# Kernel tuning notes

Hardware: AMD Instinct MI355X
Metric: run time of the kernel (lower is better)

## Reference

```python
import jax, jax.numpy as jnp
import numpy as np

NPOINT, NSAMPLE, RADIUS = 2048, 32, 0.2
EPS = 1e-5


def setup_inputs() -> dict:
    key = jax.random.key(0)
    ks = jax.random.split(key, 12)
    B, N, C = 8, 8192, 64
    mlp = [64, 64, 128]
    inp = {
        "xyz": jax.random.normal(ks[0], (B, 3, N), dtype=jnp.float32),
        "points": jax.random.normal(ks[1], (B, C, N), dtype=jnp.float32),
    }
    last = C + 3  # use_xyz concatenates 3 relative coords
    for i, out in enumerate(mlp, 1):
        inp[f"W{i}"] = jax.random.normal(ks[2 * i], (out, last), dtype=jnp.float32) / np.sqrt(last).astype(np.float32)
        inp[f"b{i}"] = jnp.zeros((out,), jnp.float32)
        inp[f"g{i}"] = jnp.ones((out,), jnp.float32)
        inp[f"be{i}"] = jnp.zeros((out,), jnp.float32)
        last = out
    return inp


def fps(xyz_t, npoint):
    """Farthest point sampling. xyz_t: (B,N,3) -> (B,npoint) int32 indices."""
    xyz_t = jax.lax.stop_gradient(xyz_t)  # indices are non-differentiable
    B, N, _ = xyz_t.shape

    def step(carry, _):
        dists, far = carry  # (B,N), (B,)
        cent = jnp.take_along_axis(xyz_t, far[:, None, None], axis=1)  # (B,1,3)
        d = jnp.sum((xyz_t - cent) ** 2, axis=-1)
        dists = jnp.minimum(dists, d)
        nf = jnp.argmax(dists, axis=-1).astype(jnp.int32)
        return (dists, nf), far

    init = (jnp.full((B, N), 1e10, xyz_t.dtype), jnp.zeros((B,), jnp.int32))
    _, idxs = jax.lax.scan(step, init, None, length=npoint)
    return jnp.transpose(idxs)  # (B, npoint)


def ball_query(xyz_t, new_xyz_t, radius, nsample):
    """First-nsample-in-radius neighbor indices, padded with first hit.
    xyz_t (B,N,3), new_xyz_t (B,M,3) -> (B,M,nsample) int32."""
    B, N, _ = xyz_t.shape
    # squared distances via gemm to avoid (B,M,N,3) intermediate
    sq = (jnp.sum(new_xyz_t ** 2, -1)[:, :, None]
          + jnp.sum(xyz_t ** 2, -1)[:, None, :]
          - 2.0 * jnp.einsum('bmd,bnd->bmn', new_xyz_t, xyz_t))  # (B,M,N)
    cand = jnp.where(sq < radius * radius, jnp.arange(N, dtype=jnp.int32), N)
    idx = jnp.sort(cand, axis=-1)[:, :, :nsample]  # first k in-radius by index order
    first = idx[:, :, :1]
    first = jnp.where(first == N, 0, first)  # guard empty groups
    idx = jnp.where(idx == N, first, idx)
    return idx


def group(feat, idx):
    """feat (B,C,N), idx (B,M,k) -> (B,C,M,k) gathered neighbor features."""
    return jnp.take_along_axis(feat[:, :, None, :], idx[:, None, :, :], axis=3)


def conv_bn_relu(x, W, b, g, be):
    """Shared 1x1 Conv2d + BatchNorm2d (batch stats, training mode) + ReLU.
    x: (B,C,M,K) -> (B,O,M,K)."""
    y = jnp.einsum('oc,bcmk->bomk', W, x) + b[None, :, None, None]
    mu = jnp.mean(y, axis=(0, 2, 3), keepdims=True)
    var = jnp.var(y, axis=(0, 2, 3), keepdims=True)
    y = (y - mu) * jax.lax.rsqrt(var + EPS)
    y = y * g[None, :, None, None] + be[None, :, None, None]
    return jax.nn.relu(y)


def reference(xyz, points, W1, b1, g1, be1, W2, b2, g2, be2, W3, b3, g3, be3):
    xyz_t = jnp.transpose(xyz, (0, 2, 1))  # (B,N,3)
    fidx = fps(xyz_t, NPOINT)  # (B,M)
    new_xyz = jnp.take_along_axis(xyz, fidx[:, None, :], axis=2)  # (B,3,M)
    idx = ball_query(xyz_t, jnp.transpose(new_xyz, (0, 2, 1)), RADIUS, NSAMPLE)  # (B,M,K)
    grouped_xyz = group(xyz, idx) - new_xyz[:, :, :, None]  # (B,3,M,K) centered
    grouped_pts = group(points, idx)  # (B,f,M,K)
    x = jnp.concatenate([grouped_xyz, grouped_pts], axis=1)  # (B,f+3,M,K)
    x = conv_bn_relu(x, W1, b1, g1, be1)
    x = conv_bn_relu(x, W2, b2, g2, be2)
    x = conv_bn_relu(x, W3, b3, g3, be3)
    new_points = jnp.max(x, axis=3)  # (B,mlp[-1],M)
    return (new_xyz, new_points)
```

## Files before the change

### kernel.cpp

```cpp
#include <hip/hip_runtime.h>

#define BB 8
#define NN 8192
#define MM 2048
#define KK 32
#define NTOT (BB*MM*KK)

#define WS_PTS_T  0
#define WS_XYZN   4194304
#define WS_IDX    5242880
#define WS_GPART  5767168
#define WS_PARAMS 6291456
#define WS_ZMAX   6292480
#define WS_ZMIN   8389632
#define WS_TOTAL  10486784

typedef float v2f __attribute__((ext_vector_type(2)));

__global__ __launch_bounds__(256) void k_transpose(const float* __restrict__ pts,
                                                   float* __restrict__ pts_t){
  __shared__ float tile[64][65];
  int bid = blockIdx.x;
  int b = bid >> 7;
  int n0 = (bid & 127) << 6;
  int tx = threadIdx.x & 63, ty = threadIdx.x >> 6;
  const float* src = pts + (size_t)b*64*NN;
  #pragma unroll
  for (int c = ty; c < 64; c += 4)
    tile[c][tx] = src[(size_t)c*NN + n0 + tx];
  __syncthreads();
  float* dst = pts_t + ((size_t)b*NN + n0)*64;
  #pragma unroll
  for (int r = ty; r < 64; r += 4)
    dst[(size_t)r*64 + tx] = tile[tx][r];
}

__global__ __launch_bounds__(256) void k_xyzn(const float* __restrict__ xyz,
                                              float4* __restrict__ xyzn){
  #pragma clang fp contract(off)
  int i = blockIdx.x*256 + threadIdx.x;
  int b = i >> 13, n = i & 8191;
  const float* p = xyz + (size_t)b*3*NN;
  float x = p[n], y = p[NN+n], z = p[2*NN+n];
  float nrm = (x*x + y*y) + z*z;
  xyzn[i] = make_float4(x, y, z, nrm);
}

#define DPPMAXF(ctrl, rmask)                                                 \
  {                                                                          \
    float s_ = __int_as_float(__builtin_amdgcn_update_dpp(                   \
        __float_as_int(m), __float_as_int(m), (ctrl), (rmask), 0xf, false)); \
    m = fmaxf(m, s_);                                                        \
  }

__global__ __launch_bounds__(256,1) void k_fps(const float* __restrict__ xyz,
                                               float* __restrict__ out_newxyz){
  #pragma clang fp contract(off)
  __shared__ float4 sp4[NN];
  __shared__ unsigned long long swk[2][4];
  int b = blockIdx.x, tid = threadIdx.x;
  const float* xb = xyz + (size_t)b*3*NN;
  int n0 = tid << 5;
  v2f px[16], py[16], pz[16], dd[16];
  const float4* xb4 = (const float4*)xb;
  #pragma unroll
  for (int q = 0; q < 8; ++q){
    float4 X = xb4[(n0>>2) + q];
    float4 Y = xb4[(NN>>2) + (n0>>2) + q];
    float4 Z = xb4[((2*NN)>>2) + (n0>>2) + q];
    px[2*q]   = (v2f){X.x, X.y}; px[2*q+1] = (v2f){X.z, X.w};
    py[2*q]   = (v2f){Y.x, Y.y}; py[2*q+1] = (v2f){Y.z, Y.w};
    pz[2*q]   = (v2f){Z.x, Z.y}; pz[2*q+1] = (v2f){Z.z, Z.w};
    dd[2*q]   = (v2f){1e10f,1e10f}; dd[2*q+1] = (v2f){1e10f,1e10f};
    sp4[n0+4*q+0] = make_float4(X.x, Y.x, Z.x, 0.f);
    sp4[n0+4*q+1] = make_float4(X.y, Y.y, Z.y, 0.f);
    sp4[n0+4*q+2] = make_float4(X.z, Y.z, Z.z, 0.f);
    sp4[n0+4*q+3] = make_float4(X.w, Y.w, Z.w, 0.f);
  }
  __syncthreads();
  float4 c0 = sp4[0];
  float cx = c0.x, cy = c0.y, cz = c0.z;
  float* ob = out_newxyz + (size_t)b*3*MM;
  int lane = tid & 63, wid = tid >> 6;
  const int JINF = 0x7fffffff;
  for (int s = 0; s < 8; ++s){
    float ox = 0.f, oy = 0.f, oz = 0.f;
    #pragma unroll 1
    for (int ti = 0; ti < 256; ++ti){
      if (tid == ti){ ox = cx; oy = cy; oz = cz; }
      v2f cvx = (v2f){cx,cx}, cvy = (v2f){cy,cy}, cvz = (v2f){cz,cz};
      #pragma unroll
      for (int g = 0; g < 16; ++g){
        v2f dx = px[g]-cvx, dy = py[g]-cvy, dz = pz[g]-cvz;
        v2f xx = dx*dx, yy = dy*dy, zz = dz*dz;
        v2f sm = xx + yy;
        v2f d  = sm + zz;
        dd[g] = __builtin_elementwise_min(dd[g], d);
      }
      v2f t8[8], t4[4], t2[2], t1;
      #pragma unroll
      for (int g = 0; g < 8; ++g) t8[g] = __builtin_elementwise_max(dd[2*g], dd[2*g+1]);
      #pragma unroll
      for (int g = 0; g < 4; ++g) t4[g] = __builtin_elementwise_max(t8[2*g], t8[2*g+1]);
      t2[0] = __builtin_elementwise_max(t4[0], t4[1]);
      t2[1] = __builtin_elementwise_max(t4[2], t4[3]);
      t1 = __builtin_elementwise_max(t2[0], t2[1]);
      float bv = fmaxf(t1.x, t1.y);
      float m = bv;
      DPPMAXF(0x111, 0xf)
      DPPMAXF(0x112, 0xf)
      DPPMAXF(0x114, 0xf)
      DPPMAXF(0x118, 0xf)
      DPPMAXF(0x142, 0xa)
      DPPMAXF(0x143, 0xc)
      float wm = __int_as_float(__builtin_amdgcn_readlane(__float_as_int(m), 63));
      unsigned long long msk = __ballot(bv == wm);
      int wl = (int)__builtin_ctzll(msk);
      int s16[16], s8[8], s4[4], s2[2];
      #pragma unroll
      for (int g = 0; g < 16; ++g){
        int j0 = (dd[g].x == bv) ? (2*g)   : JINF;
        int j1 = (dd[g].y == bv) ? (2*g+1) : JINF;
        s16[g] = min(j0, j1);
      }
      #pragma unroll
      for (int g = 0; g < 8; ++g) s8[g] = min(s16[2*g], s16[2*g+1]);
      #pragma unroll
      for (int g = 0; g < 4; ++g) s4[g] = min(s8[2*g], s8[2*g+1]);
      s2[0] = min(s4[0], s4[1]); s2[1] = min(s4[2], s4[3]);
      int bj = min(s2[0], s2[1]);
      int nwin = __builtin_amdgcn_readlane(n0 + bj, wl);
      int buf = ti & 1;
      if (lane == 0){
        unsigned long long key =
            ((unsigned long long)__float_as_uint(wm) << 32) |
            (unsigned int)(~(unsigned int)nwin);
        swk[buf][wid] = key;
      }
      __syncthreads();
      const unsigned long long* kk = swk[buf];
      unsigned long long k0=kk[0], k1=kk[1], k2=kk[2], k3=kk[3];
      unsigned long long a = (k0>k1)?k0:k1, c2 = (k2>k3)?k2:k3;
      unsigned long long kmax = (a>c2)?a:c2;
      int far = (int)(~(unsigned int)kmax) & (NN-1);
      float4 c4 = sp4[far];
      cx = c4.x; cy = c4.y; cz = c4.z;
    }
    ob[(s<<8)+tid] = ox; ob[MM+(s<<8)+tid] = oy; ob[2*MM+(s<<8)+tid] = oz;
  }
}

__global__ __launch_bounds__(256) void k_ballq(const float4* __restrict__ xyzn,
                                               const float* __restrict__ newxyz,
                                               int* __restrict__ idx){
  #pragma clang fp contract(off)
  __shared__ unsigned long long s_mask[32][129];
  __shared__ float4 s_c4[32];
  const float R2 = (float)(0.2*0.2);
  int b = blockIdx.x >> 6;
  int m0 = (blockIdx.x & 63) << 5;
  int tid = threadIdx.x, lane = tid & 63, wv = tid >> 6;
  const float* nb = newxyz + (size_t)b*3*MM;
  if (tid < 32){
    int m = m0 + tid;
    float cx = nb[m], cy = nb[MM+m], cz = nb[2*MM+m];
    float cn = (cx*cx + cy*cy) + cz*cz;
    s_c4[tid] = make_float4(cx, cy, cz, cn);
  }
  __syncthreads();
  const float4* src = xyzn + (size_t)b*NN;
  for (int ci = 0; ci < 32; ++ci){
    int ch = ci*4 + wv;
    float4 p = src[ch*64 + lane];
    #pragma unroll 8
    for (int mi = 0; mi < 32; ++mi){
      float4 c = s_c4[mi];
      float dot = (c.x*p.x + c.y*p.y) + c.z*p.z;
      float sq = (c.w + p.w) - 2.0f*dot;
      unsigned long long mk = __ballot(sq < R2);
      if (lane == 0) s_mask[mi][ch] = mk;
    }
  }
  __syncthreads();
  if (tid < 32){
    int m = m0 + tid;
    int* om = idx + ((size_t)(b*MM + m))*KK;
    int filled = 0, first = -1;
    for (int ch = 0; ch < 128 && filled < KK; ++ch){
      unsigned long long mk = s_mask[tid][ch];
      while (mk){
        int bp = __builtin_ctzll(mk);
        mk &= mk - 1;
        int j = ch*64 + bp;
        if (first < 0) first = j;
        om[filled++] = j;
        if (filled == KK) break;
      }
    }
    int pad = (first < 0) ? 0 : first;
    for (int s = filled; s < KK; ++s) om[s] = pad;
  }
}

#define XST 260
#define PST 66

__device__ __forceinline__ void gemm_step(v2f (&acc)[8][4], const float* sw,
                                          const float* sx, int c, int ob8, int pb){
  float4 X0 = *(const float4*)&sx[c*XST + pb];
  float4 X1 = *(const float4*)&sx[c*XST + pb + 4];
  v2f xv[4] = { (v2f){X0.x,X0.y}, (v2f){X0.z,X0.w},
                (v2f){X1.x,X1.y}, (v2f){X1.z,X1.w} };
  float4 W0 = *(const float4*)&sw[c*64 + ob8];
  float4 W1 = *(const float4*)&sw[c*64 + ob8 + 4];
  float ws[8] = {W0.x,W0.y,W0.z,W0.w,W1.x,W1.y,W1.z,W1.w};
  #pragma unroll
  for (int oi = 0; oi < 8; ++oi){
    v2f wv = (v2f){ws[oi], ws[oi]};
    #pragma unroll
    for (int p = 0; p < 4; ++p)
      acc[oi][p] = __builtin_elementwise_fma(wv, xv[p], acc[oi][p]);
  }
}

__device__ __forceinline__ void zero_acc(v2f (&acc)[8][4]){
  #pragma unroll
  for (int oi = 0; oi < 8; ++oi)
    #pragma unroll
    for (int p = 0; p < 4; ++p) acc[oi][p] = (v2f){0.f, 0.f};
}

__device__ __forceinline__ void gather_col(float* sx, const float* pts_t,
    const float4* xyzn, const float* nb, const int* idx, int b, int bid, int tid){
  int m0 = (bid & 255) << 3;
  int m = m0 + (tid >> 5), k = tid & 31;
  int j = idx[((size_t)(b*MM + m))*KK + k];
  float4 P = xyzn[(size_t)b*NN + j];
  sx[0*XST + tid] = P.x - nb[m];
  sx[1*XST + tid] = P.y - nb[MM+m];
  sx[2*XST + tid] = P.z - nb[2*MM+m];
  const float4* pf = (const float4*)(pts_t + ((size_t)b*NN + j)*64);
  #pragma unroll
  for (int c4 = 0; c4 < 16; ++c4){
    float4 v = pf[c4];
    sx[(3+4*c4+0)*XST + tid] = v.x;
    sx[(3+4*c4+1)*XST + tid] = v.y;
    sx[(3+4*c4+2)*XST + tid] = v.z;
    sx[(3+4*c4+3)*XST + tid] = v.w;
  }
}

__device__ __forceinline__ void bnrelu_tile(v2f (&acc)[8][4], const float* sA,
                                            const float* sC, int ob8){
  v2f Z = (v2f){0.f, 0.f};
  #pragma unroll
  for (int oi = 0; oi < 8; ++oi){
    v2f Av = (v2f){sA[ob8+oi], sA[ob8+oi]};
    v2f Cv = (v2f){sC[ob8+oi], sC[ob8+oi]};
    #pragma unroll
    for (int p = 0; p < 4; ++p)
      acc[oi][p] = __builtin_elementwise_max(
          __builtin_elementwise_fma(Av, acc[oi][p], Cv), Z);
  }
}

__device__ __forceinline__ void stash_tile(const v2f (&acc)[8][4], float* sx,
                                           int ob8, int pb){
  #pragma unroll
  for (int oi = 0; oi < 8; ++oi){
    *(float4*)&sx[(ob8+oi)*XST + pb] =
        make_float4(acc[oi][0].x, acc[oi][0].y, acc[oi][1].x, acc[oi][1].y);
    *(float4*)&sx[(ob8+oi)*XST + pb + 4] =
        make_float4(acc[oi][2].x, acc[oi][2].y, acc[oi][3].x, acc[oi][3].y);
  }
}

__device__ __forceinline__ void tile_stats(const v2f (&acc)[8][4], float* s_pp,
    float* gpart, int ob8, int pg, int tid, int bid, int nch_base){
  #pragma unroll
  for (int oi = 0; oi < 8; ++oi){
    float a0x=acc[oi][0].x, a0y=acc[oi][0].y, a0z=acc[oi][1].x, a0w=acc[oi][1].y;
    float a1x=acc[oi][2].x, a1y=acc[oi][2].y, a1z=acc[oi][3].x, a1w=acc[oi][3].y;
    float s  = ((a0x+a0y)+(a0z+a0w)) + ((a1x+a1y)+(a1z+a1w));
    float q2 = ((a0x*a0x + a0y*a0y) + (a0z*a0z + a0w*a0w))
             + ((a1x*a1x + a1y*a1y) + (a1z*a1z + a1w*a1w));
    int o = ob8 + oi;
    s_pp[o*PST + pg*2 + 0] = s;
    s_pp[o*PST + pg*2 + 1] = q2;
  }
  __syncthreads();
  if (tid < 128){
    int o = tid >> 1, st = tid & 1;
    float S = 0.f;
    #pragma unroll 8
    for (int q = 0; q < 32; ++q) S += s_pp[o*PST + q*2 + st];
    gpart[(size_t)(st*128 + nch_base + o)*2048 + bid] = S;
  }
}

__global__ __launch_bounds__(256,1) void k_conv1_stats(const float* __restrict__ pts_t,
    const float4* __restrict__ xyzn, const float* __restrict__ newxyz,
    const int* __restrict__ idx, const float* __restrict__ W1, float* __restrict__ gpart){
  __shared__ float s_w1[67*64];
  __shared__ float s_x[67*XST];
  int tid = threadIdx.x;
  for (int i = tid; i < 67*64; i += 256){ int c = i>>6, o = i&63; s_w1[i] = W1[o*67 + c]; }
  int bid = blockIdx.x, b = bid >> 8;
  const float* nb = newxyz + (size_t)b*3*MM;
  gather_col(s_x, pts_t, xyzn, nb, idx, b, bid, tid);
  __syncthreads();
  int oq = tid & 7, pg = tid >> 3;
  int ob8 = oq*8, pb = pg*8;
  v2f acc[8][4];
  zero_acc(acc);
  for (int c = 0; c < 67; ++c) gemm_step(acc, s_w1, s_x, c, ob8, pb);
  __syncthreads();
  tile_stats(acc, s_x, gpart, ob8, pg, tid, bid, 0);
}

__global__ __launch_bounds__(256,1) void k_conv2_stats(const float* __restrict__ pts_t,
    const float4* __restrict__ xyzn, const float* __restrict__ newxyz,
    const int* __restrict__ idx, const float* __restrict__ W1, const float* __restrict__ W2,
    const float* __restrict__ params1, float* __restrict__ gpart){
  __shared__ float s_w1[67*64];
  __shared__ float s_w2[64*64];
  __shared__ float s_p[128];
  __shared__ float s_x[67*XST];
  int tid = threadIdx.x;
  for (int i = tid; i < 67*64; i += 256){ int c = i>>6, o = i&63; s_w1[i] = W1[o*67 + c]; }
  for (int i = tid; i < 64*64; i += 256){ int c = i>>6, o = i&63; s_w2[i] = W2[o*64 + c]; }
  if (tid < 64){ s_p[tid] = params1[tid]; s_p[64+tid] = params1[128+tid]; }
  int bid = blockIdx.x, b = bid >> 8;
  const float* nb = newxyz + (size_t)b*3*MM;
  gather_col(s_x, pts_t, xyzn, nb, idx, b, bid, tid);
  __syncthreads();
  int oq = tid & 7, pg = tid >> 3;
  int ob8 = oq*8, pb = pg*8;
  v2f acc[8][4];
  zero_acc(acc);
  for (int c = 0; c < 67; ++c) gemm_step(acc, s_w1, s_x, c, ob8, pb);
  bnrelu_tile(acc, s_p, s_p+64, ob8);
  __syncthreads();
  stash_tile(acc, s_x, ob8, pb);
  __syncthreads();
  zero_acc(acc);
  for (int c = 0; c < 64; ++c) gemm_step(acc, s_w2, s_x, c, ob8, pb);
  __syncthreads();
  tile_stats(acc, s_x, gpart, ob8, pg, tid, bid, 0);
}

__global__ __launch_bounds__(256) void k_bnfin(const float* __restrict__ gpart,
    const float* __restrict__ g, const float* __restrict__ be, float* __restrict__ params){
  int o = blockIdx.x, t = threadIdx.x;
  double s = 0.0, sq = 0.0;
  for (int i = t; i < 2048; i += 256){
    s  += (double)gpart[(size_t)o*2048 + i];
    sq += (double)gpart[(size_t)(128+o)*2048 + i];
  }
  __shared__ double ds[256], dq[256];
  ds[t] = s; dq[t] = sq; __syncthreads();
  for (int off = 128; off > 0; off >>= 1){
    if (t < off){ ds[t] += ds[t+off]; dq[t] += dq[t+off]; }
    __syncthreads();
  }
  if (t == 0){
    double mu = ds[0] / (double)NTOT;
    double var = dq[0] / (double)NTOT - mu*mu;
    float A = g[o] / sqrtf((float)var + 1e-5f);
    float Cc = be[o] - (float)mu * A;
    params[o] = A; params[128+o] = Cc;
  }
}

__global__ __launch_bounds__(256,1) void k_conv3(const float* __restrict__ pts_t,
    const float4* __restrict__ xyzn, const float* __restrict__ newxyz,
    const int* __restrict__ idx, const float* __restrict__ W1, const float* __restrict__ W2,
    const float* __restrict__ W3, const float* __restrict__ params1,
    const float* __restrict__ params2, float* __restrict__ gpart,
    float* __restrict__ zmax, float* __restrict__ zmin){
  __shared__ float s_w1[67*64];
  __shared__ float s_w2[64*64];
  __shared__ float s_w3[64*128];
  __shared__ float s_p[256];
  __shared__ float s_x[67*XST];
  __shared__ float s_sm[8*128*2];
  int tid = threadIdx.x;
  for (int i = tid; i < 67*64; i += 256){ int c = i>>6, o = i&63; s_w1[i] = W1[o*67 + c]; }
  for (int i = tid; i < 64*64; i += 256){ int c = i>>6, o = i&63; s_w2[i] = W2[o*64 + c]; }
  for (int i = tid; i < 64*128; i += 256){ int c = i>>7, o = i&127; s_w3[c*128+o] = W3[o*64 + c]; }
  if (tid < 64){
    s_p[tid]      = params1[tid];     s_p[64+tid]  = params1[128+tid];
    s_p[128+tid]  = params2[tid];     s_p[192+tid] = params2[128+tid];
  }
  int bid = blockIdx.x, b = bid >> 8, m0 = (bid & 255) << 3;
  const float* nb = newxyz + (size_t)b*3*MM;
  gather_col(s_x, pts_t, xyzn, nb, idx, b, bid, tid);
  __syncthreads();
  int oq = tid & 7, pg = tid >> 3;
  int ob8 = oq*8, pb = pg*8;
  v2f acc[8][4];
  zero_acc(acc);
  for (int c = 0; c < 67; ++c) gemm_step(acc, s_w1, s_x, c, ob8, pb);
  bnrelu_tile(acc, s_p, s_p+64, ob8);
  __syncthreads();
  stash_tile(acc, s_x, ob8, pb);
  __syncthreads();
  zero_acc(acc);
  for (int c = 0; c < 64; ++c) gemm_step(acc, s_w2, s_x, c, ob8, pb);
  bnrelu_tile(acc, s_p+128, s_p+192, ob8);
  __syncthreads();
  stash_tile(acc, s_x, ob8, pb);
  __syncthreads();
  int ml = tid >> 5, og = tid & 31;
  v2f accK[4][16];
  #pragma unroll
  for (int oo = 0; oo < 4; ++oo)
    #pragma unroll
    for (int p = 0; p < 16; ++p) accK[oo][p] = (v2f){0.f, 0.f};
  for (int c = 0; c < 64; ++c){
    float4 w = *(const float4*)&s_w3[c*128 + og*4];
    v2f w0 = (v2f){w.x,w.x}, w1 = (v2f){w.y,w.y};
    v2f w2 = (v2f){w.z,w.z}, w3v = (v2f){w.w,w.w};
    #pragma unroll
    for (int q = 0; q < 8; ++q){
      float4 xv = *(const float4*)&s_x[c*XST + ml*32 + q*4];
      v2f xa = (v2f){xv.x, xv.y}, xb2 = (v2f){xv.z, xv.w};
      accK[0][2*q]   = __builtin_elementwise_fma(w0,  xa,  accK[0][2*q]);
      accK[0][2*q+1] = __builtin_elementwise_fma(w0,  xb2, accK[0][2*q+1]);
      accK[1][2*q]   = __builtin_elementwise_fma(w1,  xa,  accK[1][2*q]);
      accK[1][2*q+1] = __builtin_elementwise_fma(w1,  xb2, accK[1][2*q+1]);
      accK[2][2*q]   = __builtin_elementwise_fma(w2,  xa,  accK[2][2*q]);
      accK[2][2*q+1] = __builtin_elementwise_fma(w2,  xb2, accK[2][2*q+1]);
      accK[3][2*q]   = __builtin_elementwise_fma(w3v, xa,  accK[3][2*q]);
      accK[3][2*q+1] = __builtin_elementwise_fma(w3v, xb2, accK[3][2*q+1]);
    }
  }
  int m = m0 + ml;
  #pragma unroll
  for (int oo = 0; oo < 4; ++oo){
    float mx = -3.4e38f, mn = 3.4e38f, s = 0.f, sq = 0.f;
    #pragma unroll
    for (int p = 0; p < 16; ++p){
      float v0 = accK[oo][p].x, v1 = accK[oo][p].y;
      mx = fmaxf(mx, v0); mx = fmaxf(mx, v1);
      mn = fminf(mn, v0); mn = fminf(mn, v1);
      s += v0; s += v1;
      sq = fmaf(v0, v0, sq); sq = fmaf(v1, v1, sq);
    }
    int o = og*4 + oo;
    zmax[((size_t)(b*128 + o))*MM + m] = mx;
    zmin[((size_t)(b*128 + o))*MM + m] = mn;
    s_sm[(ml*128+o)*2] = s; s_sm[(ml*128+o)*2+1] = sq;
  }
  __syncthreads();
  {
    int o = tid >> 1, st = tid & 1;
    float S = 0.f;
    #pragma unroll
    for (int mm = 0; mm < 8; ++mm) S += s_sm[(mm*128+o)*2 + st];
    gpart[(size_t)(st*128+o)*2048 + bid] = S;
  }
}

__global__ __launch_bounds__(256) void k_out(const float* __restrict__ zmax,
    const float* __restrict__ zmin, const float* __restrict__ params3,
    float* __restrict__ out){
  int i = blockIdx.x*256 + threadIdx.x;
  int o = (i >> 11) & 127;
  float A = params3[o], Cc = params3[128+o];
  float v = (A >= 0.f) ? fmaf(A, zmax[i], Cc) : fmaf(A, zmin[i], Cc);
  out[49152 + i] = fmaxf(v, 0.f);
}

extern "C" void kernel_launch(void* const* d_in, const int* in_sizes, int n_in,
                              void* d_out, int out_size, void* d_ws, size_t ws_size,
                              hipStream_t stream){
  const float* xyz    = (const float*)d_in[0];
  const float* points = (const float*)d_in[1];
  const float* W1  = (const float*)d_in[2];
  const float* g1  = (const float*)d_in[4];
  const float* be1 = (const float*)d_in[5];
  const float* W2  = (const float*)d_in[6];
  const float* g2  = (const float*)d_in[8];
  const float* be2 = (const float*)d_in[9];
  const float* W3  = (const float*)d_in[10];
  const float* g3  = (const float*)d_in[12];
  const float* be3 = (const float*)d_in[13];

  if (ws_size < (size_t)WS_TOTAL * sizeof(float)) return;

  float*  ws     = (float*)d_ws;
  float*  pts_t  = ws + WS_PTS_T;
  float4* xyzn   = (float4*)(ws + WS_XYZN);
  int*    idx    = (int*)(ws + WS_IDX);
  float*  gpart  = ws + WS_GPART;
  float*  params = ws + WS_PARAMS;
  float*  zmax   = ws + WS_ZMAX;
  float*  zmin   = ws + WS_ZMIN;
  float*  out    = (float*)d_out;
  float*  newxyz = out;

  hipLaunchKernelGGL(k_fps,       dim3(8),    dim3(256), 0, stream, xyz, newxyz);
  hipLaunchKernelGGL(k_transpose, dim3(1024), dim3(256), 0, stream, points, pts_t);
  hipLaunchKernelGGL(k_xyzn,      dim3(256),  dim3(256), 0, stream, xyz, xyzn);
  hipLaunchKernelGGL(k_ballq,     dim3(512),  dim3(256), 0, stream, xyzn, newxyz, idx);
  hipLaunchKernelGGL(k_conv1_stats, dim3(2048), dim3(256), 0, stream,
                     pts_t, xyzn, newxyz, idx, W1, gpart);
  hipLaunchKernelGGL(k_bnfin, dim3(64), dim3(256), 0, stream, gpart, g1, be1, params+0);
  hipLaunchKernelGGL(k_conv2_stats, dim3(2048), dim3(256), 0, stream,
                     pts_t, xyzn, newxyz, idx, W1, W2, params+0, gpart);
  hipLaunchKernelGGL(k_bnfin, dim3(64), dim3(256), 0, stream, gpart, g2, be2, params+256);
  hipLaunchKernelGGL(k_conv3, dim3(2048), dim3(256), 0, stream,
                     pts_t, xyzn, newxyz, idx, W1, W2, W3, params+0, params+256,
                     gpart, zmax, zmin);
  hipLaunchKernelGGL(k_bnfin, dim3(128), dim3(256), 0, stream, gpart, g3, be3, params+512);
  hipLaunchKernelGGL(k_out, dim3(8192), dim3(256), 0, stream, zmax, zmin, params+512, out);
}
```

Measured before the change: 2.635 ms.

## Double conv block threads to 512 and streamline FPS per-step argmax reduction

The three fused conv kernels now run 512 threads per block. Each thread computes half as many points per output group, the gather is split across two thread halves by channel range, and the conv3 output tile is repartitioned to two channels per thread. The FPS inner loop folds the running max into the distance update and finds the first matching index with a reverse conditional scan instead of separate reduction trees. The aim is more waves per CU to hide the latency of the gemm and gather phases, and a shorter serial FPS step. The cost is more sync participants and a smaller register tile, so each thread does less reuse.

After: 2.568 ms. 1.03x faster.

```diff
diff --git a/kernel.cpp b/kernel.cpp
--- a/kernel.cpp
+++ b/kernel.cpp
@@ -82,30 +82,24 @@
   float cx = c0.x, cy = c0.y, cz = c0.z;
   float* ob = out_newxyz + (size_t)b*3*MM;
   int lane = tid & 63, wid = tid >> 6;
-  const int JINF = 0x7fffffff;
   for (int s = 0; s < 8; ++s){
     float ox = 0.f, oy = 0.f, oz = 0.f;
     #pragma unroll 1
     for (int ti = 0; ti < 256; ++ti){
       if (tid == ti){ ox = cx; oy = cy; oz = cz; }
       v2f cvx = (v2f){cx,cx}, cvy = (v2f){cy,cy}, cvz = (v2f){cz,cz};
+      v2f bv2 = (v2f){-1.f,-1.f};
       #pragma unroll
       for (int g = 0; g < 16; ++g){
         v2f dx = px[g]-cvx, dy = py[g]-cvy, dz = pz[g]-cvz;
         v2f xx = dx*dx, yy = dy*dy, zz = dz*dz;
         v2f sm = xx + yy;
         v2f d  = sm + zz;
-        dd[g] = __builtin_elementwise_min(dd[g], d);
+        v2f nd = __builtin_elementwise_min(dd[g], d);
+        dd[g] = nd;
+        bv2 = __builtin_elementwise_max(bv2, nd);
       }
-      v2f t8[8], t4[4], t2[2], t1;
-      #pragma unroll
-      for (int g = 0; g < 8; ++g) t8[g] = __builtin_elementwise_max(dd[2*g], dd[2*g+1]);
-      #pragma unroll
-      for (int g = 0; g < 4; ++g) t4[g] = __builtin_elementwise_max(t8[2*g], t8[2*g+1]);
-      t2[0] = __builtin_elementwise_max(t4[0], t4[1]);
-      t2[1] = __builtin_elementwise_max(t4[2], t4[3]);
-      t1 = __builtin_elementwise_max(t2[0], t2[1]);
-      float bv = fmaxf(t1.x, t1.y);
+      float bv = fmaxf(bv2.x, bv2.y);
       float m = bv;
       DPPMAXF(0x111, 0xf)
       DPPMAXF(0x112, 0xf)
@@ -116,19 +110,12 @@
       float wm = __int_as_float(__builtin_amdgcn_readlane(__float_as_int(m), 63));
       unsigned long long msk = __ballot(bv == wm);
       int wl = (int)__builtin_ctzll(msk);
-      int s16[16], s8[8], s4[4], s2[2];
+      int bj = 0;
       #pragma unroll
-      for (int g = 0; g < 16; ++g){
-        int j0 = (dd[g].x == bv) ? (2*g)   : JINF;
-        int j1 = (dd[g].y == bv) ? (2*g+1) : JINF;
-        s16[g] = min(j0, j1);
+      for (int g = 15; g >= 0; --g){
+        if (dd[g].y == bv) bj = 2*g+1;
+        if (dd[g].x == bv) bj = 2*g;
       }
-      #pragma unroll
-      for (int g = 0; g < 8; ++g) s8[g] = min(s16[2*g], s16[2*g+1]);
-      #pragma unroll
-      for (int g = 0; g < 4; ++g) s4[g] = min(s8[2*g], s8[2*g+1]);
-      s2[0] = min(s4[0], s4[1]); s2[1] = min(s4[2], s4[3]);
-      int bj = min(s2[0], s2[1]);
       int nwin = __builtin_amdgcn_readlane(n0 + bj, wl);
       int buf = ti & 1;
       if (lane == 0){
@@ -203,122 +190,122 @@
 }
 
 #define XST 260
-#define PST 66
-
-__device__ __forceinline__ void gemm_step(v2f (&acc)[8][4], const float* sw,
+#define PSTW 130
+
+__device__ __forceinline__ void gemm_step(v2f (&acc)[8][2], const float* sw,
                                           const float* sx, int c, int ob8, int pb){
-  float4 X0 = *(const float4*)&sx[c*XST + pb];
-  float4 X1 = *(const float4*)&sx[c*XST + pb + 4];
-  v2f xv[4] = { (v2f){X0.x,X0.y}, (v2f){X0.z,X0.w},
-                (v2f){X1.x,X1.y}, (v2f){X1.z,X1.w} };
+  float4 X = *(const float4*)&sx[c*XST + pb];
+  v2f x0 = (v2f){X.x, X.y}, x1 = (v2f){X.z, X.w};
   float4 W0 = *(const float4*)&sw[c*64 + ob8];
   float4 W1 = *(const float4*)&sw[c*64 + ob8 + 4];
   float ws[8] = {W0.x,W0.y,W0.z,W0.w,W1.x,W1.y,W1.z,W1.w};
   #pragma unroll
   for (int oi = 0; oi < 8; ++oi){
     v2f wv = (v2f){ws[oi], ws[oi]};
-    #pragma unroll
-    for (int p = 0; p < 4; ++p)
-      acc[oi][p] = __builtin_elementwise_fma(wv, xv[p], acc[oi][p]);
-  }
-}
-
-__device__ __forceinline__ void zero_acc(v2f (&acc)[8][4]){
-  #pragma unroll
-  for (int oi = 0; oi < 8; ++oi)
-    #pragma unroll
-    for (int p = 0; p < 4; ++p) acc[oi][p] = (v2f){0.f, 0.f};
+    acc[oi][0] = __builtin_elementwise_fma(wv, x0, acc[oi][0]);
+    acc[oi][1] = __builtin_elementwise_fma(wv, x1, acc[oi][1]);
+  }
+}
+
+__device__ __forceinline__ void zero_acc(v2f (&acc)[8][2]){
+  #pragma unroll
+  for (int oi = 0; oi < 8; ++oi){ acc[oi][0] = (v2f){0.f,0.f}; acc[oi][1] = (v2f){0.f,0.f}; }
 }
 
 __device__ __forceinline__ void gather_col(float* sx, const float* pts_t,
     const float4* xyzn, const float* nb, const int* idx, int b, int bid, int tid){
+  int pos = tid & 255, half = tid >> 8;
   int m0 = (bid & 255) << 3;
-  int m = m0 + (tid >> 5), k = tid & 31;
+  int m = m0 + (pos >> 5), k = pos & 31;
   int j = idx[((size_t)(b*MM + m))*KK + k];
-  float4 P = xyzn[(size_t)b*NN + j];
-  sx[0*XST + tid] = P.x - nb[m];
-  sx[1*XST + tid] = P.y - nb[MM+m];
-  sx[2*XST + tid] = P.z - nb[2*MM+m];
   const float4* pf = (const float4*)(pts_t + ((size_t)b*NN + j)*64);
-  #pragma unroll
-  for (int c4 = 0; c4 < 16; ++c4){
-    float4 v = pf[c4];
-    sx[(3+4*c4+0)*XST + tid] = v.x;
-    sx[(3+4*c4+1)*XST + tid] = v.y;
-    sx[(3+4*c4+2)*XST + tid] = v.z;
-    sx[(3+4*c4+3)*XST + tid] = v.w;
-  }
-}
-
-__device__ __forceinline__ void bnrelu_tile(v2f (&acc)[8][4], const float* sA,
+  if (half == 0){
+    float4 P = xyzn[(size_t)b*NN + j];
+    sx[0*XST + pos] = P.x - nb[m];
+    sx[1*XST + pos] = P.y - nb[MM+m];
+    sx[2*XST + pos] = P.z - nb[2*MM+m];
+    #pragma unroll
+    for (int c4 = 0; c4 < 8; ++c4){
+      float4 v = pf[c4];
+      sx[(3+4*c4+0)*XST + pos] = v.x;
+      sx[(3+4*c4+1)*XST + pos] = v.y;
+      sx[(3+4*c4+2)*XST + pos] = v.z;
+      sx[(3+4*c4+3)*XST + pos] = v.w;
+    }
+  } else {
+    #pragma unroll
+    for (int c4 = 8; c4 < 16; ++c4){
+      float4 v = pf[c4];
+      sx[(3+4*c4+0)*XST + pos] = v.x;
+      sx[(3+4*c4+1)*XST + pos] = v.y;
+      sx[(3+4*c4+2)*XST + pos] = v.z;
+      sx[(3+4*c4+3)*XST + pos] = v.w;
+    }
+  }
+}
+
+__device__ __forceinline__ void bnrelu_tile(v2f (&acc)[8][2], const float* sA,
                                             const float* sC, int ob8){
   v2f Z = (v2f){0.f, 0.f};
   #pragma unroll
   for (int oi = 0; oi < 8; ++oi){
     v2f Av = (v2f){sA[ob8+oi], sA[ob8+oi]};
     v2f Cv = (v2f){sC[ob8+oi], sC[ob8+oi]};
-    #pragma unroll
-    for (int p = 0; p < 4; ++p)
-      acc[oi][p] = __builtin_elementwise_max(
-          __builtin_elementwise_fma(Av, acc[oi][p], Cv), Z);
-  }
-}
-
-__device__ __forceinline__ void stash_tile(const v2f (&acc)[8][4], float* sx,
+    acc[oi][0] = __builtin_elementwise_max(__builtin_elementwise_fma(Av, acc[oi][0], Cv), Z);
+    acc[oi][1] = __builtin_elementwise_max(__builtin_elementwise_fma(Av, acc[oi][1], Cv), Z);
+  }
+}
+
+__device__ __forceinline__ void stash_tile(const v2f (&acc)[8][2], float* sx,
                                            int ob8, int pb){
   #pragma unroll
-  for (int oi = 0; oi < 8; ++oi){
+  for (int oi = 0; oi < 8; ++oi)
     *(float4*)&sx[(ob8+oi)*XST + pb] =
         make_float4(acc[oi][0].x, acc[oi][0].y, acc[oi][1].x, acc[oi][1].y);
-    *(float4*)&sx[(ob8+oi)*XST + pb + 4] =
-        make_float4(acc[oi][2].x, acc[oi][2].y, acc[oi][3].x, acc[oi][3].y);
-  }
-}
-
-__device__ __forceinline__ void tile_stats(const v2f (&acc)[8][4], float* s_pp,
-    float* gpart, int ob8, int pg, int tid, int bid, int nch_base){
+}
+
+__device__ __forceinline__ void tile_stats(const v2f (&acc)[8][2], float* s_pp,
+    float* gpart, int ob8, int pg, int tid, int bid){
   #pragma unroll
   for (int oi = 0; oi < 8; ++oi){
-    float a0x=acc[oi][0].x, a0y=acc[oi][0].y, a0z=acc[oi][1].x, a0w=acc[oi][1].y;
-    float a1x=acc[oi][2].x, a1y=acc[oi][2].y, a1z=acc[oi][3].x, a1w=acc[oi][3].y;
-    float s  = ((a0x+a0y)+(a0z+a0w)) + ((a1x+a1y)+(a1z+a1w));
-    float q2 = ((a0x*a0x + a0y*a0y) + (a0z*a0z + a0w*a0w))
-             + ((a1x*a1x + a1y*a1y) + (a1z*a1z + a1w*a1w));
+    v2f a0 = acc[oi][0], a1 = acc[oi][1];
+    float s  = (a0.x + a0.y) + (a1.x + a1.y);
+    float q2 = (a0.x*a0.x + a0.y*a0.y) + (a1.x*a1.x + a1.y*a1.y);
     int o = ob8 + oi;
-    s_pp[o*PST + pg*2 + 0] = s;
-    s_pp[o*PST + pg*2 + 1] = q2;
+    s_pp[o*PSTW + pg*2 + 0] = s;
+    s_pp[o*PSTW + pg*2 + 1] = q2;
   }
   __syncthreads();
   if (tid < 128){
     int o = tid >> 1, st = tid & 1;
     float S = 0.f;
     #pragma unroll 8
-    for (int q = 0; q < 32; ++q) S += s_pp[o*PST + q*2 + st];
-    gpart[(size_t)(st*128 + nch_base + o)*2048 + bid] = S;
-  }
-}
-
-__global__ __launch_bounds__(256,1) void k_conv1_stats(const float* __restrict__ pts_t,
+    for (int q = 0; q < 64; ++q) S += s_pp[o*PSTW + q*2 + st];
+    gpart[(size_t)(st*128 + o)*2048 + bid] = S;
+  }
+}
+
+__global__ __launch_bounds__(512,1) void k_conv1_stats(const float* __restrict__ pts_t,
     const float4* __restrict__ xyzn, const float* __restrict__ newxyz,
     const int* __restrict__ idx, const float* __restrict__ W1, float* __restrict__ gpart){
   __shared__ float s_w1[67*64];
   __shared__ float s_x[67*XST];
   int tid = threadIdx.x;
-  for (int i = tid; i < 67*64; i += 256){ int c = i>>6, o = i&63; s_w1[i] = W1[o*67 + c]; }
+  for (int i = tid; i < 67*64; i += 512){ int c = i>>6, o = i&63; s_w1[i] = W1[o*67 + c]; }
   int bid = blockIdx.x, b = bid >> 8;
   const float* nb = newxyz + (size_t)b*3*MM;
   gather_col(s_x, pts_t, xyzn, nb, idx, b, bid, tid);
   __syncthreads();
   int oq = tid & 7, pg = tid >> 3;
-  int ob8 = oq*8, pb = pg*8;
-  v2f acc[8][4];
+  int ob8 = oq*8, pb = pg*4;
+  v2f acc[8][2];
   zero_acc(acc);
   for (int c = 0; c < 67; ++c) gemm_step(acc, s_w1, s_x, c, ob8, pb);
   __syncthreads();
-  tile_stats(acc, s_x, gpart, ob8, pg, tid, bid, 0);
-}
-
-__global__ __launch_bounds__(256,1) void k_conv2_stats(const float* __restrict__ pts_t,
+  tile_stats(acc, s_x, gpart, ob8, pg, tid, bid);
+}
+
+__global__ __launch_bounds__(512,1) void k_conv2_stats(const float* __restrict__ pts_t,
     const float4* __restrict__ xyzn, const float* __restrict__ newxyz,
     const int* __restrict__ idx, const float* __restrict__ W1, const float* __restrict__ W2,
     const float* __restrict__ params1, float* __restrict__ gpart){
@@ -327,16 +314,16 @@
   __shared__ float s_p[128];
   __shared__ float s_x[67*XST];
   int tid = threadIdx.x;
-  for (int i = tid; i < 67*64; i += 256){ int c = i>>6, o = i&63; s_w1[i] = W1[o*67 + c]; }
-  for (int i = tid; i < 64*64; i += 256){ int c = i>>6, o = i&63; s_w2[i] = W2[o*64 + c]; }
+  for (int i = tid; i < 67*64; i += 512){ int c = i>>6, o = i&63; s_w1[i] = W1[o*67 + c]; }
+  for (int i = tid; i < 64*64; i += 512){ int c = i>>6, o = i&63; s_w2[i] = W2[o*64 + c]; }
   if (tid < 64){ s_p[tid] = params1[tid]; s_p[64+tid] = params1[128+tid]; }
   int bid = blockIdx.x, b = bid >> 8;
   const float* nb = newxyz + (size_t)b*3*MM;
   gather_col(s_x, pts_t, xyzn, nb, idx, b, bid, tid);
   __syncthreads();
   int oq = tid & 7, pg = tid >> 3;
-  int ob8 = oq*8, pb = pg*8;
-  v2f acc[8][4];
+  int ob8 = oq*8, pb = pg*4;
+  v2f acc[8][2];
   zero_acc(acc);
   for (int c = 0; c < 67; ++c) gemm_step(acc, s_w1, s_x, c, ob8, pb);
   bnrelu_tile(acc, s_p, s_p+64, ob8);
@@ -346,7 +333,7 @@
   zero_acc(acc);
   for (int c = 0; c < 64; ++c) gemm_step(acc, s_w2, s_x, c, ob8, pb);
   __syncthreads();
-  tile_stats(acc, s_x, gpart, ob8, pg, tid, bid, 0);
+  tile_stats(acc, s_x, gpart, ob8, pg, tid, bid);
 }
 
 __global__ __launch_bounds__(256) void k_bnfin(const float* __restrict__ gpart,
@@ -372,7 +359,7 @@
   }
 }
 
-__global__ __launch_bounds__(256,1) void k_conv3(const float* __restrict__ pts_t,
+__global__ __launch_bounds__(512,1) void k_conv3(const float* __restrict__ pts_t,
     const float4* __restrict__ xyzn, const float* __restrict__ newxyz,
     const int* __restrict__ idx, const float* __restrict__ W1, const float* __restrict__ W2,
     const float* __restrict__ W3, const float* __restrict__ params1,
@@ -385,9 +372,9 @@
   __shared__ float s_x[67*XST];
   __shared__ float s_sm[8*128*2];
   int tid = threadIdx.x;
-  for (int i = tid; i < 67*64; i += 256){ int c = i>>6, o = i&63; s_w1[i] = W1[o*67 + c]; }
-  for (int i = tid; i < 64*64; i += 256){ int c = i>>6, o = i&63; s_w2[i] = W2[o*64 + c]; }
-  for (int i = tid; i < 64*128; i += 256){ int c = i>>7, o = i&127; s_w3[c*128+o] = W3[o*64 + c]; }
+  for (int i = tid; i < 67*64; i += 512){ int c = i>>6, o = i&63; s_w1[i] = W1[o*67 + c]; }
+  for (int i = tid; i < 64*64; i += 512){ int c = i>>6, o = i&63; s_w2[i] = W2[o*64 + c]; }
+  for (int i = tid; i < 64*128; i += 512){ int c = i>>7, o = i&127; s_w3[c*128+o] = W3[o*64 + c]; }
   if (tid < 64){
     s_p[tid]      = params1[tid];     s_p[64+tid]  = params1[128+tid];
     s_p[128+tid]  = params2[tid];     s_p[192+tid] = params2[128+tid];
@@ -397,8 +384,8 @@
   gather_col(s_x, pts_t, xyzn, nb, idx, b, bid, tid);
   __syncthreads();
   int oq = tid & 7, pg = tid >> 3;
-  int ob8 = oq*8, pb = pg*8;
-  v2f acc[8][4];
+  int ob8 = oq*8, pb = pg*4;
+  v2f acc[8][2];
   zero_acc(acc);
   for (int c = 0; c < 67; ++c) gemm_step(acc, s_w1, s_x, c, ob8, pb);
   bnrelu_tile(acc, s_p, s_p+64, ob8);
@@ -411,33 +398,28 @@
   __syncthreads();
   stash_tile(acc, s_x, ob8, pb);
   __syncthreads();
-  int ml = tid >> 5, og = tid & 31;
-  v2f accK[4][16];
-  #pragma unroll
-  for (int oo = 0; oo < 4; ++oo)
+  int ml = tid >> 6, og = tid & 63;
+  v2f accK[2][16];
+  #pragma unroll
+  for (int oo = 0; oo < 2; ++oo)
     #pragma unroll
     for (int p = 0; p < 16; ++p) accK[oo][p] = (v2f){0.f, 0.f};
   for (int c = 0; c < 64; ++c){
-    float4 w = *(const float4*)&s_w3[c*128 + og*4];
-    v2f w0 = (v2f){w.x,w.x}, w1 = (v2f){w.y,w.y};
-    v2f w2 = (v2f){w.z,w.z}, w3v = (v2f){w.w,w.w};
+    v2f w = *(const v2f*)&s_w3[c*128 + og*2];
+    v2f w0 = (v2f){w.x, w.x}, w1 = (v2f){w.y, w.y};
     #pragma unroll
     for (int q = 0; q < 8; ++q){
       float4 xv = *(const float4*)&s_x[c*XST + ml*32 + q*4];
       v2f xa = (v2f){xv.x, xv.y}, xb2 = (v2f){xv.z, xv.w};
-      accK[0][2*q]   = __builtin_elementwise_fma(w0,  xa,  accK[0][2*q]);
-      accK[0][2*q+1] = __builtin_elementwise_fma(w0,  xb2, accK[0][2*q+1]);
-      accK[1][2*q]   = __builtin_elementwise_fma(w1,  xa,  accK[1][2*q]);
-      accK[1][2*q+1] = __builtin_elementwise_fma(w1,  xb2, accK[1][2*q+1]);
-      accK[2][2*q]   = __builtin_elementwise_fma(w2,  xa,  accK[2][2*q]);
-      accK[2][2*q+1] = __builtin_elementwise_fma(w2,  xb2, accK[2][2*q+1]);
-      accK[3][2*q]   = __builtin_elementwise_fma(w3v, xa,  accK[3][2*q]);
-      accK[3][2*q+1] = __builtin_elementwise_fma(w3v, xb2, accK[3][2*q+1]);
+      accK[0][2*q]   = __builtin_elementwise_fma(w0, xa,  accK[0][2*q]);
+      accK[0][2*q+1] = __builtin_elementwise_fma(w0, xb2, accK[0][2*q+1]);
+      accK[1][2*q]   = __builtin_elementwise_fma(w1, xa,  accK[1][2*q]);
+      accK[1][2*q+1] = __builtin_elementwise_fma(w1, xb2, accK[1][2*q+1]);
     }
   }
   int m = m0 + ml;
   #pragma unroll
-  for (int oo = 0; oo < 4; ++oo){
+  for (int oo = 0; oo < 2; ++oo){
     float mx = -3.4e38f, mn = 3.4e38f, s = 0.f, sq = 0.f;
     #pragma unroll
     for (int p = 0; p < 16; ++p){
@@ -447,13 +429,13 @@
       s += v0; s += v1;
       sq = fmaf(v0, v0, sq); sq = fmaf(v1, v1, sq);
     }
-    int o = og*4 + oo;
+    int o = og*2 + oo;
     zmax[((size_t)(b*128 + o))*MM + m] = mx;
     zmin[((size_t)(b*128 + o))*MM + m] = mn;
     s_sm[(ml*128+o)*2] = s; s_sm[(ml*128+o)*2+1] = sq;
   }
   __syncthreads();
-  {
+  if (tid < 256){
     int o = tid >> 1, st = tid & 1;
     float S = 0.f;
     #pragma unroll
@@ -504,13 +486,13 @@
   hipLaunchKernelGGL(k_transpose, dim3(1024), dim3(256), 0, stream, points, pts_t);
   hipLaunchKernelGGL(k_xyzn,      dim3(256),  dim3(256), 0, stream, xyz, xyzn);
   hipLaunchKernelGGL(k_ballq,     dim3(512),  dim3(256), 0, stream, xyzn, newxyz, idx);
-  hipLaunchKernelGGL(k_conv1_stats, dim3(2048), dim3(256), 0, stream,
+  hipLaunchKernelGGL(k_conv1_stats, dim3(2048), dim3(512), 0, stream,
                      pts_t, xyzn, newxyz, idx, W1, gpart);
   hipLaunchKernelGGL(k_bnfin, dim3(64), dim3(256), 0, stream, gpart, g1, be1, params+0);
-  hipLaunchKernelGGL(k_conv2_stats, dim3(2048), dim3(256), 0, stream,
+  hipLaunchKernelGGL(k_conv2_stats, dim3(2048), dim3(512), 0, stream,
                      pts_t, xyzn, newxyz, idx, W1, W2, params+0, gpart);
   hipLaunchKernelGGL(k_bnfin, dim3(64), dim3(256), 0, stream, gpart, g2, be2, params+256);
-  hipLaunchKernelGGL(k_conv3, dim3(2048), dim3(256), 0, stream,
+  hipLaunchKernelGGL(k_conv3, dim3(2048), dim3(512), 0, stream,
                      pts_t, xyzn, newxyz, idx, W1, W2, W3, params+0, params+256,
                      gpart, zmax, zmin);
   hipLaunchKernelGGL(k_bnfin, dim3(128), dim3(256), 0, stream, gpart, g3, be3, params+512);
```
